# Kernel tuning notes

Hardware: AMD Instinct MI355X
Metric: run time of the kernel (lower is better)

The kernel has to match this reference:

```python
import jax, jax.numpy as jnp
import numpy as np

N = 200000
NSEG = 2048  # number of graphs in the batch (fixed for jit)
EPS = 1e-6


def setup_inputs() -> dict:
    key = jax.random.key(0)
    k1, k2, k3 = jax.random.split(key, 3)
    s = jax.random.normal(k1, (N, 256), dtype=jnp.float32)
    v = jax.random.normal(k2, (N, 3, 128), dtype=jnp.float32)
    weight = jnp.ones((256,), dtype=jnp.float32)
    bias = jnp.zeros((256,), dtype=jnp.float32)
    batch = jnp.sort(jax.random.randint(k3, (N,), 0, NSEG, dtype=jnp.int32))
    return {"s": s, "v": v, "weight": weight, "bias": bias, "batch": batch}


def _scatter_mean(x, batch, cnt):
    # x: [N, ...], batch: [N] int, cnt: [NSEG] float (clamped >= 1)
    sums = jax.ops.segment_sum(x, batch, num_segments=NSEG)
    return sums / cnt.reshape((NSEG,) + (1,) * (x.ndim - 1))


def reference(s, v, weight, bias, batch):
    cnt = jnp.maximum(
        jax.ops.segment_sum(jnp.ones((s.shape[0],), dtype=s.dtype), batch, num_segments=NSEG),
        1.0,
    )
    # scalar branch: per-graph mean of per-node channel-means
    smean = _scatter_mean(s.mean(axis=-1, keepdims=True), batch, cnt)  # [NSEG,1]
    s_c = s - smean[batch]
    var = _scatter_mean((s_c * s_c).mean(axis=-1, keepdims=True), batch, cnt)  # [NSEG,1]
    var = jnp.maximum(var, EPS)
    # NOTE: original divides by var (not sqrt(var)) — faithful to source
    sout = s_c / var[batch] * weight + bias
    # vector branch: per-graph mean of mean squared vector norm
    vmean_node = (v * v).sum(axis=1, keepdims=True).mean(axis=-1, keepdims=True)  # [N,1,1]
    vmean = _scatter_mean(vmean_node, batch, cnt)  # [NSEG,1,1]
    vmean = jnp.maximum(vmean, EPS)
    vout = v / vmean[batch]
    return sout, vout
```

## Files before the change

kernel.cpp:

```cpp
#include <hip/hip_runtime.h>

#define NSEG 2048
#define EPS 1e-6f

__device__ __forceinline__ float wave_reduce(float x) {
    #pragma unroll
    for (int off = 32; off > 0; off >>= 1) x += __shfl_down(x, off, 64);
    return x;
}

__global__ void zero_ws_kernel(float* __restrict__ ws, int n) {
    int i = blockIdx.x * blockDim.x + threadIdx.x;
    if (i < n) ws[i] = 0.0f;
}

__global__ void pass1_kernel(const float* __restrict__ s,
                             const float* __restrict__ v,
                             const int* __restrict__ batch,
                             float* __restrict__ ws, int n) {
    const int lane  = threadIdx.x & 63;
    const int wave  = (blockIdx.x * blockDim.x + threadIdx.x) >> 6;
    const int nwav  = (gridDim.x * blockDim.x) >> 6;
    const int chunk = (n + nwav - 1) / nwav;
    const int start = wave * chunk;
    const int end   = min(start + chunk, n);
    if (start >= end) return;

    float* sum_s = ws;
    float* sum_q = ws + NSEG;
    float* sum_v = ws + 2 * NSEG;
    float* cntp  = ws + 3 * NSEG;

    float ls = 0.0f, lq = 0.0f, lv = 0.0f;
    int run = 0;
    int cur = -1;

    for (int i = start; i < end; ++i) {
        const int g = batch[i];
        if (g != cur) {
            if (run > 0) {
                float rs = wave_reduce(ls);
                float rq = wave_reduce(lq);
                float rv = wave_reduce(lv);
                if (lane == 0) {
                    atomicAdd(&sum_s[cur], rs);
                    atomicAdd(&sum_q[cur], rq);
                    atomicAdd(&sum_v[cur], rv);
                    atomicAdd(&cntp[cur], (float)run);
                }
            }
            ls = lq = lv = 0.0f;
            run = 0;
            cur = g;
        }
        const float4 x = ((const float4*)(s + (size_t)i * 256))[lane];
        ls += x.x + x.y + x.z + x.w;
        lq += x.x * x.x + x.y * x.y + x.z * x.z + x.w * x.w;
        const float4 y = ((const float4*)(v + (size_t)i * 384))[lane];
        lv += y.x * y.x + y.y * y.y + y.z * y.z + y.w * y.w;
        const float2 z = ((const float2*)(v + (size_t)i * 384 + 256))[lane];
        lv += z.x * z.x + z.y * z.y;
        ++run;
    }
    if (run > 0) {
        float rs = wave_reduce(ls);
        float rq = wave_reduce(lq);
        float rv = wave_reduce(lv);
        if (lane == 0) {
            atomicAdd(&sum_s[cur], rs);
            atomicAdd(&sum_q[cur], rq);
            atomicAdd(&sum_v[cur], rv);
            atomicAdd(&cntp[cur], (float)run);
        }
    }
}

__global__ void finalize_kernel(float* __restrict__ ws) {
    int g = blockIdx.x * blockDim.x + threadIdx.x;
    if (g >= NSEG) return;
    float n   = fmaxf(ws[3 * NSEG + g], 1.0f);
    float sm  = ws[g] / (256.0f * n);
    float es2 = ws[NSEG + g] / (256.0f * n);
    float var = fmaxf(es2 - sm * sm, EPS);
    float vm  = fmaxf(ws[2 * NSEG + g] / (128.0f * n), EPS);
    ws[4 * NSEG + g] = sm;
    ws[5 * NSEG + g] = 1.0f / var;
    ws[6 * NSEG + g] = 1.0f / vm;
}

__global__ void pass2_kernel(const float* __restrict__ s,
                             const float* __restrict__ v,
                             const int* __restrict__ batch,
                             const float* __restrict__ weight,
                             const float* __restrict__ bias,
                             const float* __restrict__ ws,
                             float* __restrict__ out, int n) {
    const int lane  = threadIdx.x & 63;
    const int wave  = (blockIdx.x * blockDim.x + threadIdx.x) >> 6;
    const int nwav  = (gridDim.x * blockDim.x) >> 6;
    const int chunk = (n + nwav - 1) / nwav;
    const int start = wave * chunk;
    const int end   = min(start + chunk, n);
    if (start >= end) return;

    const float* smean = ws + 4 * NSEG;
    const float* ivar  = ws + 5 * NSEG;
    const float* ivmn  = ws + 6 * NSEG;

    const float4 w4 = ((const float4*)weight)[lane];
    const float4 b4 = ((const float4*)bias)[lane];

    float* sout = out;
    float* vout = out + (size_t)n * 256;

    for (int i = start; i < end; ++i) {
        const int g = batch[i];
        const float sm = smean[g];
        const float iv = ivar[g];
        const float im = ivmn[g];

        const float4 x = ((const float4*)(s + (size_t)i * 256))[lane];
        float4 o;
        o.x = (x.x - sm) * iv * w4.x + b4.x;
        o.y = (x.y - sm) * iv * w4.y + b4.y;
        o.z = (x.z - sm) * iv * w4.z + b4.z;
        o.w = (x.w - sm) * iv * w4.w + b4.w;
        ((float4*)(sout + (size_t)i * 256))[lane] = o;

        float4 y = ((const float4*)(v + (size_t)i * 384))[lane];
        y.x *= im; y.y *= im; y.z *= im; y.w *= im;
        ((float4*)(vout + (size_t)i * 384))[lane] = y;

        float2 z = ((const float2*)(v + (size_t)i * 384 + 256))[lane];
        z.x *= im; z.y *= im;
        ((float2*)(vout + (size_t)i * 384 + 256))[lane] = z;
    }
}

extern "C" void kernel_launch(void* const* d_in, const int* in_sizes, int n_in,
                              void* d_out, int out_size, void* d_ws, size_t ws_size,
                              hipStream_t stream) {
    const float* s      = (const float*)d_in[0];
    const float* v      = (const float*)d_in[1];
    const float* weight = (const float*)d_in[2];
    const float* bias   = (const float*)d_in[3];
    const int*   batch  = (const int*)d_in[4];
    float* out = (float*)d_out;
    float* ws  = (float*)d_ws;

    const int n = in_sizes[0] / 256;

    zero_ws_kernel<<<(4 * NSEG + 255) / 256, 256, 0, stream>>>(ws, 4 * NSEG);

    pass1_kernel<<<1024, 256, 0, stream>>>(s, v, batch, ws, n);

    finalize_kernel<<<(NSEG + 255) / 256, 256, 0, stream>>>(ws);

    pass2_kernel<<<1024, 256, 0, stream>>>(s, v, batch, weight, bias, ws, out, n);
}
```

Baseline: 934.1 us.

## Fuse passes into one segment-per-block kernel with binary-searched boundaries

Replaces the four-kernel pipeline (zero, atomic stats pass, finalize, normalize pass) with a single kernel where each block owns four consecutive segments. It finds segment boundaries by binary search on the sorted batch array, reduces the statistics across its waves in shared memory, then immediately normalizes the same rows. Because the rows were just read, the second read can hit in cache, and the global atomics and extra launches go away. Outputs use nontemporal stores. The trade-offs are a grid of only 512 blocks, block-wide barriers per segment, and load imbalance if segment sizes vary.

Result: faster. 895.7 us (-4.1%).

```diff
diff --git a/kernel.cpp b/kernel.cpp
--- a/kernel.cpp
+++ b/kernel.cpp
@@ -2,6 +2,12 @@
 
 #define NSEG 2048
 #define EPS 1e-6f
+#define GRID 512
+#define SPB (NSEG / GRID)
+#define NWAVE 4
+
+typedef float f4 __attribute__((ext_vector_type(4)));
+typedef float f2 __attribute__((ext_vector_type(2)));
 
 __device__ __forceinline__ float wave_reduce(float x) {
     #pragma unroll
@@ -9,131 +15,96 @@
     return x;
 }
 
-__global__ void zero_ws_kernel(float* __restrict__ ws, int n) {
-    int i = blockIdx.x * blockDim.x + threadIdx.x;
-    if (i < n) ws[i] = 0.0f;
-}
+__global__ __launch_bounds__(256) void fused_kernel(
+        const float* __restrict__ s,
+        const float* __restrict__ v,
+        const int* __restrict__ batch,
+        const float* __restrict__ weight,
+        const float* __restrict__ bias,
+        float* __restrict__ out, int n) {
+    const int lane = threadIdx.x & 63;
+    const int w    = threadIdx.x >> 6;
 
-__global__ void pass1_kernel(const float* __restrict__ s,
-                             const float* __restrict__ v,
-                             const int* __restrict__ batch,
-                             float* __restrict__ ws, int n) {
-    const int lane  = threadIdx.x & 63;
-    const int wave  = (blockIdx.x * blockDim.x + threadIdx.x) >> 6;
-    const int nwav  = (gridDim.x * blockDim.x) >> 6;
-    const int chunk = (n + nwav - 1) / nwav;
-    const int start = wave * chunk;
-    const int end   = min(start + chunk, n);
-    if (start >= end) return;
+    __shared__ int   sstart[SPB + 1];
+    __shared__ float red_s[NWAVE], red_q[NWAVE], red_v[NWAVE];
+    __shared__ float p_sm, p_iv, p_im;
 
-    float* sum_s = ws;
-    float* sum_q = ws + NSEG;
-    float* sum_v = ws + 2 * NSEG;
-    float* cntp  = ws + 3 * NSEG;
+    const int g0 = blockIdx.x * SPB;
 
-    float ls = 0.0f, lq = 0.0f, lv = 0.0f;
-    int run = 0;
-    int cur = -1;
+    if (threadIdx.x <= SPB) {
+        const int target = g0 + threadIdx.x;
+        int lo = 0, hi = n;
+        while (lo < hi) {
+            const int mid = (lo + hi) >> 1;
+            if (batch[mid] < target) lo = mid + 1; else hi = mid;
+        }
+        sstart[threadIdx.x] = lo;
+    }
 
-    for (int i = start; i < end; ++i) {
-        const int g = batch[i];
-        if (g != cur) {
-            if (run > 0) {
-                float rs = wave_reduce(ls);
-                float rq = wave_reduce(lq);
-                float rv = wave_reduce(lv);
-                if (lane == 0) {
-                    atomicAdd(&sum_s[cur], rs);
-                    atomicAdd(&sum_q[cur], rq);
-                    atomicAdd(&sum_v[cur], rv);
-                    atomicAdd(&cntp[cur], (float)run);
-                }
-            }
-            ls = lq = lv = 0.0f;
-            run = 0;
-            cur = g;
-        }
-        const float4 x = ((const float4*)(s + (size_t)i * 256))[lane];
-        ls += x.x + x.y + x.z + x.w;
-        lq += x.x * x.x + x.y * x.y + x.z * x.z + x.w * x.w;
-        const float4 y = ((const float4*)(v + (size_t)i * 384))[lane];
-        lv += y.x * y.x + y.y * y.y + y.z * y.z + y.w * y.w;
-        const float2 z = ((const float2*)(v + (size_t)i * 384 + 256))[lane];
-        lv += z.x * z.x + z.y * z.y;
-        ++run;
-    }
-    if (run > 0) {
-        float rs = wave_reduce(ls);
-        float rq = wave_reduce(lq);
-        float rv = wave_reduce(lv);
-        if (lane == 0) {
-            atomicAdd(&sum_s[cur], rs);
-            atomicAdd(&sum_q[cur], rq);
-            atomicAdd(&sum_v[cur], rv);
-            atomicAdd(&cntp[cur], (float)run);
-        }
-    }
-}
-
-__global__ void finalize_kernel(float* __restrict__ ws) {
-    int g = blockIdx.x * blockDim.x + threadIdx.x;
-    if (g >= NSEG) return;
-    float n   = fmaxf(ws[3 * NSEG + g], 1.0f);
-    float sm  = ws[g] / (256.0f * n);
-    float es2 = ws[NSEG + g] / (256.0f * n);
-    float var = fmaxf(es2 - sm * sm, EPS);
-    float vm  = fmaxf(ws[2 * NSEG + g] / (128.0f * n), EPS);
-    ws[4 * NSEG + g] = sm;
-    ws[5 * NSEG + g] = 1.0f / var;
-    ws[6 * NSEG + g] = 1.0f / vm;
-}
-
-__global__ void pass2_kernel(const float* __restrict__ s,
-                             const float* __restrict__ v,
-                             const int* __restrict__ batch,
-                             const float* __restrict__ weight,
-                             const float* __restrict__ bias,
-                             const float* __restrict__ ws,
-                             float* __restrict__ out, int n) {
-    const int lane  = threadIdx.x & 63;
-    const int wave  = (blockIdx.x * blockDim.x + threadIdx.x) >> 6;
-    const int nwav  = (gridDim.x * blockDim.x) >> 6;
-    const int chunk = (n + nwav - 1) / nwav;
-    const int start = wave * chunk;
-    const int end   = min(start + chunk, n);
-    if (start >= end) return;
-
-    const float* smean = ws + 4 * NSEG;
-    const float* ivar  = ws + 5 * NSEG;
-    const float* ivmn  = ws + 6 * NSEG;
-
-    const float4 w4 = ((const float4*)weight)[lane];
-    const float4 b4 = ((const float4*)bias)[lane];
+    const f4 w4 = ((const f4*)weight)[lane];
+    const f4 b4 = ((const f4*)bias)[lane];
 
     float* sout = out;
     float* vout = out + (size_t)n * 256;
 
-    for (int i = start; i < end; ++i) {
-        const int g = batch[i];
-        const float sm = smean[g];
-        const float iv = ivar[g];
-        const float im = ivmn[g];
+    __syncthreads();
 
-        const float4 x = ((const float4*)(s + (size_t)i * 256))[lane];
-        float4 o;
-        o.x = (x.x - sm) * iv * w4.x + b4.x;
-        o.y = (x.y - sm) * iv * w4.y + b4.y;
-        o.z = (x.z - sm) * iv * w4.z + b4.z;
-        o.w = (x.w - sm) * iv * w4.w + b4.w;
-        ((float4*)(sout + (size_t)i * 256))[lane] = o;
+    for (int sl = 0; sl < SPB; ++sl) {
+        const int i0 = sstart[sl];
+        const int i1 = sstart[sl + 1];
+        if (i0 >= i1) continue;
 
-        float4 y = ((const float4*)(v + (size_t)i * 384))[lane];
-        y.x *= im; y.y *= im; y.z *= im; y.w *= im;
-        ((float4*)(vout + (size_t)i * 384))[lane] = y;
+        float ls = 0.0f, lq = 0.0f, lv = 0.0f;
+        #pragma unroll 2
+        for (int i = i0 + w; i < i1; i += NWAVE) {
+            const f4 x = ((const f4*)(s + (size_t)i * 256))[lane];
+            ls += x.x + x.y + x.z + x.w;
+            lq += x.x * x.x + x.y * x.y + x.z * x.z + x.w * x.w;
+            const f4 y = ((const f4*)(v + (size_t)i * 384))[lane];
+            lv += y.x * y.x + y.y * y.y + y.z * y.z + y.w * y.w;
+            const f2 z = ((const f2*)(v + (size_t)i * 384 + 256))[lane];
+            lv += z.x * z.x + z.y * z.y;
+        }
+        const float rs = wave_reduce(ls);
+        const float rq = wave_reduce(lq);
+        const float rv = wave_reduce(lv);
+        if (lane == 0) { red_s[w] = rs; red_q[w] = rq; red_v[w] = rv; }
+        __syncthreads();
 
-        float2 z = ((const float2*)(v + (size_t)i * 384 + 256))[lane];
-        z.x *= im; z.y *= im;
-        ((float2*)(vout + (size_t)i * 384 + 256))[lane] = z;
+        if (threadIdx.x == 0) {
+            const float S = red_s[0] + red_s[1] + red_s[2] + red_s[3];
+            const float Q = red_q[0] + red_q[1] + red_q[2] + red_q[3];
+            const float V = red_v[0] + red_v[1] + red_v[2] + red_v[3];
+            const float nn  = (float)(i1 - i0);
+            const float sm  = S / (256.0f * nn);
+            const float var = fmaxf(Q / (256.0f * nn) - sm * sm, EPS);
+            const float vm  = fmaxf(V / (128.0f * nn), EPS);
+            p_sm = sm;
+            p_iv = 1.0f / var;
+            p_im = 1.0f / vm;
+        }
+        __syncthreads();
+
+        const float sm = p_sm, iv = p_iv, im = p_im;
+
+        #pragma unroll 2
+        for (int i = i0 + w; i < i1; i += NWAVE) {
+            const f4 x = ((const f4*)(s + (size_t)i * 256))[lane];
+            f4 o;
+            o.x = (x.x - sm) * iv * w4.x + b4.x;
+            o.y = (x.y - sm) * iv * w4.y + b4.y;
+            o.z = (x.z - sm) * iv * w4.z + b4.z;
+            o.w = (x.w - sm) * iv * w4.w + b4.w;
+            __builtin_nontemporal_store(o, (f4*)(sout + (size_t)i * 256) + lane);
+
+            f4 y = ((const f4*)(v + (size_t)i * 384))[lane];
+            y.x *= im; y.y *= im; y.z *= im; y.w *= im;
+            __builtin_nontemporal_store(y, (f4*)(vout + (size_t)i * 384) + lane);
+
+            f2 z = ((const f2*)(v + (size_t)i * 384 + 256))[lane];
+            z.x *= im; z.y *= im;
+            __builtin_nontemporal_store(z, (f2*)(vout + (size_t)i * 384 + 256) + lane);
+        }
     }
 }
 
@@ -146,15 +117,8 @@
     const float* bias   = (const float*)d_in[3];
     const int*   batch  = (const int*)d_in[4];
     float* out = (float*)d_out;
-    float* ws  = (float*)d_ws;
 
     const int n = in_sizes[0] / 256;
 
-    zero_ws_kernel<<<(4 * NSEG + 255) / 256, 256, 0, stream>>>(ws, 4 * NSEG);
-
-    pass1_kernel<<<1024, 256, 0, stream>>>(s, v, batch, ws, n);
-
-    finalize_kernel<<<(NSEG + 255) / 256, 256, 0, stream>>>(ws);
-
-    pass2_kernel<<<1024, 256, 0, stream>>>(s, v, batch, weight, bias, ws, out, n);
+    fused_kernel<<<GRID, 256, 0, stream>>>(s, v, batch, weight, bias, out, n);
 }
```
